# Optimization experiments

Measured on AMD Instinct MI355X. Metric: run time of the kernel, lower is better.

The kernel has to match this reference:

```python
import jax, jax.numpy as jnp
import numpy as np

B, N, DH, DG, HID, K_STEPS, CURV = 256, 2048, 128, 256, 256, 2, 1.0
SC = CURV ** 0.5
SCALE = 1.0 / (DH ** 0.5)
LN_EPS = 1e-5


def _artanh(x):
    return jnp.arctanh(jnp.clip(x, -1.0 + 1e-5, 1.0 - 1e-5))


def logmap0(x, sc=SC):
    n = jnp.maximum(jnp.linalg.norm(x, axis=-1, keepdims=True), 1e-7)
    return x * (_artanh(sc * n) / (sc * n))


def expmap0(v, sc=SC):
    n = jnp.maximum(jnp.linalg.norm(v, axis=-1, keepdims=True), 1e-7)
    return v * (jnp.tanh(sc * n) / (sc * n))


def setup_inputs() -> dict:
    key = jax.random.key(0)
    ks = jax.random.split(key, 16)

    def lin(k, out_d, in_d):
        return (jax.random.normal(k, (out_d, in_d), jnp.float32) * (in_d ** -0.5))

    demo_hyp = expmap0(0.1 * jax.random.normal(ks[0], (B, N, DH), jnp.float32))
    rho_g = jax.random.normal(ks[1], (B, DG), jnp.float32)
    return {
        "demo_hyp": demo_hyp,
        "rho_g": rho_g,
        "seed_g_w": lin(ks[2], DH, DG),
        "seed_g_b": jnp.zeros((DH,), jnp.float32),
        "seed_d_w": lin(ks[3], DH, DH),
        "pool_wq_w": lin(ks[4], DH, DH),
        "pool_wk_w": lin(ks[5], DH, DH),
        "pool_wv_w": lin(ks[6], DH, DH),
        "q_u_w": lin(ks[7], DH, DH),
        "q_g_w": lin(ks[8], DH, DG),
        "q_g_b": jnp.zeros((DH,), jnp.float32),
        "kv_w": lin(ks[9], DH, DH),
        "mlp_w1": lin(ks[10], HID, DH),
        "mlp_b1": jnp.zeros((HID,), jnp.float32),
        "mlp_w2": lin(ks[11], DH, HID),
        "mlp_b2": jnp.zeros((DH,), jnp.float32),
        "ln_g": jnp.ones((DH,), jnp.float32),
        "ln_b": jnp.zeros((DH,), jnp.float32),
    }


def reference(demo_hyp, rho_g, seed_g_w, seed_g_b, seed_d_w,
              pool_wq_w, pool_wk_w, pool_wv_w, q_u_w, q_g_w, q_g_b,
              kv_w, mlp_w1, mlp_b1, mlp_w2, mlp_b2, ln_g, ln_b):
    demo_tan = logmap0(demo_hyp)                       # (B,N,Dh)

    # seed: attention-pool demos with rho_g query
    q_seed = rho_g @ seed_g_w.T + seed_g_b             # (B,Dh)
    qk = q_seed @ pool_wq_w.T                          # (B,Dh)
    Kp = demo_tan @ pool_wk_w.T                        # (B,N,Dh)
    a = jax.nn.softmax(jnp.einsum('bd,bnd->bn', qk, Kp) * SCALE, axis=-1)
    Vp = demo_tan @ pool_wv_w.T
    pooled = jnp.einsum('bn,bnd->bd', a, Vp)           # (B,Dh)
    u = expmap0(q_seed + pooled @ seed_d_w.T)

    for _ in range(K_STEPS):
        u_tan = logmap0(u)
        mu = jnp.mean(u_tan, axis=-1, keepdims=True)
        var = jnp.var(u_tan, axis=-1, keepdims=True)
        u_tan = (u_tan - mu) * jax.lax.rsqrt(var + LN_EPS) * ln_g + ln_b
        q = u_tan @ q_u_w.T + rho_g @ q_g_w.T + q_g_b
        Kmat = demo_tan @ kv_w.T                       # keys == values
        att = jax.nn.softmax(jnp.einsum('bd,bnd->bn', q, Kmat) * SCALE, axis=-1)
        delta = jnp.einsum('bn,bnd->bd', att, Kmat)
        upd = jax.nn.gelu(delta @ mlp_w1.T + mlp_b1, approximate=False) @ mlp_w2.T + mlp_b2
        u = expmap0(u_tan + upd)
    return u
```

## Files before the change

### kernel.cpp

```cpp
#include <hip/hip_runtime.h>
#include <hip/hip_fp16.h>
#include <cstddef>
#include <cstdint>

#define B 256
#define N 2048
#define DH 128
#define DG 256
#define HID 256
#define WAVES 8
#define TPB (WAVES * 64)
#define RPI (WAVES * 8)
#define KIT (N / RPI)
#define SCALE 0.08838834764831845f
#define LN_EPS 1e-5f
#define TAN_NORM_MAX 6.2f


__device__ __forceinline__ float artanh_clip(float a) {
  a = fminf(a, 1.0f - 1e-5f);
  return 0.5f * __logf((1.0f + a) / (1.0f - a));
}

__device__ __forceinline__ float logmap_scale(float n2) {
  float nc = fmaxf(sqrtf(n2), 1e-7f);
  return artanh_clip(nc) / nc;
}

__device__ __forceinline__ float row16_sum(float x) {
  x += __int_as_float(__builtin_amdgcn_update_dpp(0, __float_as_int(x), 0x128, 0xF, 0xF, true));
  x += __int_as_float(__builtin_amdgcn_update_dpp(0, __float_as_int(x), 0x124, 0xF, 0xF, true));
  x += __int_as_float(__builtin_amdgcn_update_dpp(0, __float_as_int(x), 0x122, 0xF, 0xF, true));
  x += __int_as_float(__builtin_amdgcn_update_dpp(0, __float_as_int(x), 0x121, 0xF, 0xF, true));
  return x;
}

__device__ __forceinline__ float wave_allsum(float v) {
#pragma unroll
  for (int m = 1; m < 64; m <<= 1) v += __shfl_xor(v, m);
  return v;
}

__device__ __forceinline__ float dot128(const float* __restrict__ wrow,
                                        const float* __restrict__ x) {
  const float4* a = (const float4*)wrow;
  const float4* v = (const float4*)x;
  float s = 0.f;
#pragma unroll
  for (int j = 0; j < 32; ++j) {
    float4 u = a[j], b = v[j];
    s += u.x * b.x + u.y * b.y + u.z * b.z + u.w * b.w;
  }
  return s;
}

__device__ __forceinline__ float dot256(const float* __restrict__ wrow,
                                        const float* __restrict__ x) {
  const float4* a = (const float4*)wrow;
  const float4* v = (const float4*)x;
  float s = 0.f;
#pragma unroll
  for (int j = 0; j < 64; ++j) {
    float4 u = a[j], b = v[j];
    s += u.x * b.x + u.y * b.y + u.z * b.z + u.w * b.w;
  }
  return s;
}


__global__ __launch_bounds__(TPB, 1) void fused_refiner(
    const float* __restrict__ demo, const float* __restrict__ rho,
    const float* __restrict__ seed_g_w, const float* __restrict__ seed_g_b,
    const float* __restrict__ seed_d_w, const float* __restrict__ pool_wq_w,
    const float* __restrict__ pool_wk_w, const float* __restrict__ pool_wv_w,
    const float* __restrict__ q_u_w, const float* __restrict__ q_g_w,
    const float* __restrict__ q_g_b, const float* __restrict__ kv_w,
    const float* __restrict__ mlp_w1, const float* __restrict__ mlp_b1,
    const float* __restrict__ mlp_w2, const float* __restrict__ mlp_b2,
    const float* __restrict__ ln_g, const float* __restrict__ ln_b,
    __half* __restrict__ ycache, float* __restrict__ out) {
  const int b = blockIdx.x;
  const int tid = threadIdx.x;
  const int w = tid >> 6;
  const int lane = tid & 63;
  const int g = lane >> 4;
  const int il = lane & 15;

  __shared__ __align__(16) float s_rho[DG];
  __shared__ __align__(16) float s_x[DH];
  __shared__ __align__(16) float s_y[DH];
  __shared__ __align__(16) float s_h[HID];
  __shared__ __align__(16) float s_ut[DH];
  __shared__ __align__(16) float s_qseed[DH];
  __shared__ __align__(16) float s_qvec[DH];
  __shared__ __align__(16) float s_fold[WAVES][DH];
  __shared__ float s_l[WAVES];
  __shared__ float s_red[WAVES];
  __shared__ float s_Mb;

  auto bsumAll = [&](float v) -> float {
    v = wave_allsum(v);
    if (lane == 0) s_red[w] = v;
    __syncthreads();
    float r = s_red[0] + s_red[1] + s_red[2] + s_red[3] +
              s_red[4] + s_red[5] + s_red[6] + s_red[7];
    __syncthreads();
    return r;
  };

  auto ln_query = [&](float v) {
    float n2 = bsumAll(tid < DH ? v * v : 0.f);
    float u = 0.f, ut = 0.f;
    if (tid < DH) {
      float nc = fmaxf(sqrtf(n2), 1e-7f);
      u = v * (tanhf(nc) / nc);
    }
    float nu2 = bsumAll(tid < DH ? u * u : 0.f);
    if (tid < DH) {
      float nuc = fmaxf(sqrtf(nu2), 1e-7f);
      ut = u * (artanh_clip(nuc) / nuc);
    }
    float mu = bsumAll(tid < DH ? ut : 0.f) * (1.0f / DH);
    float d = ut - mu;
    float var = bsumAll(tid < DH ? d * d : 0.f) * (1.0f / DH);
    if (tid < DH) {
      float y = d * rsqrtf(var + LN_EPS) * ln_g[tid] + ln_b[tid];
      s_ut[tid] = y;
      s_x[tid] = y;
    }
    __syncthreads();
    if (tid < DH) {
      s_y[tid] = q_g_b[tid] + dot128(q_u_w + (size_t)tid * DH, s_x) +
                 dot256(q_g_w + (size_t)tid * DG, s_rho);
    }
    __syncthreads();
    float qp = 0.f;
    if (tid < DH) {
#pragma unroll 8
      for (int i = 0; i < DH; ++i) qp += kv_w[i * DH + tid] * s_y[i];
      s_qvec[tid] = qp;
    }
    float qn2 = bsumAll(tid < DH ? qp * qp : 0.f);
    if (tid == 0) s_Mb = SCALE * TAN_NORM_MAX * sqrtf(qn2);
    __syncthreads();
  };

  if (tid < DG) s_rho[tid] = rho[(size_t)b * DG + tid];
  __syncthreads();
  if (tid < DH) {
    float qs = seed_g_b[tid] + dot256(seed_g_w + (size_t)tid * DG, s_rho);
    s_qseed[tid] = qs;
    s_x[tid] = qs;
  }
  __syncthreads();
  if (tid < DH) s_y[tid] = dot128(pool_wq_w + (size_t)tid * DH, s_x);
  __syncthreads();
  float qp0 = 0.f;
  if (tid < DH) {
#pragma unroll 8
    for (int i = 0; i < DH; ++i) qp0 += pool_wk_w[i * DH + tid] * s_y[i];
    s_qvec[tid] = qp0;
  }
  float qn2 = bsumAll(tid < DH ? qp0 * qp0 : 0.f);
  if (tid == 0) s_Mb = SCALE * TAN_NORM_MAX * sqrtf(qn2);
  __syncthreads();

  const float* demo_b = demo + (size_t)b * N * DH;
  __half* yc_b = ycache + (size_t)b * N * DH;

  for (int pass = 0; pass < 3; ++pass) {
    const float4 qv0 = *(const float4*)&s_qvec[il * 4];
    const float4 qv1 = *(const float4*)&s_qvec[64 + il * 4];
    const float Mb = s_Mb;

    float lsum = 0.f;
    float4 accL = make_float4(0.f, 0.f, 0.f, 0.f);
    float4 accH = make_float4(0.f, 0.f, 0.f, 0.f);

    if (pass == 0) {
      const float* p = demo_b + (size_t)(w * 8 + g) * DH + il * 4;
      __half* yw = yc_b + (size_t)(w * 8 + g) * DH + (size_t)il * 8;

      float4 A1[4], A2[4], B1[4], B2[4];
#pragma unroll
      for (int j = 0; j < 3; ++j) {
        const float* pj = p + (size_t)j * RPI * DH;
        A1[j] = *(const float4*)(pj);
        A2[j] = *(const float4*)(pj + 64);
        B1[j] = *(const float4*)(pj + 4 * DH);
        B2[j] = *(const float4*)(pj + 4 * DH + 64);
      }

      for (int kk = 0; kk < KIT; kk += 4) {
#pragma unroll
        for (int j = 0; j < 4; ++j) {
          const int k = kk + j;
          const int jn = (j + 3) & 3;
          if (k + 3 < KIT) {
            const float* pn = p + (size_t)(k + 3) * RPI * DH;
            A1[jn] = *(const float4*)(pn);
            A2[jn] = *(const float4*)(pn + 64);
            B1[jn] = *(const float4*)(pn + 4 * DH);
            B2[jn] = *(const float4*)(pn + 4 * DH + 64);
          }
          float4 ca1 = A1[j], ca2 = A2[j], cb1 = B1[j], cb2 = B2[j];
          {
            float dd = qv0.x * ca1.x + qv0.y * ca1.y + qv0.z * ca1.z + qv0.w * ca1.w +
                       qv1.x * ca2.x + qv1.y * ca2.y + qv1.z * ca2.z + qv1.w * ca2.w;
            float n2 = ca1.x * ca1.x + ca1.y * ca1.y + ca1.z * ca1.z + ca1.w * ca1.w +
                       ca2.x * ca2.x + ca2.y * ca2.y + ca2.z * ca2.z + ca2.w * ca2.w;
            dd = row16_sum(dd);
            n2 = row16_sum(n2);
            float tsv = logmap_scale(n2);
            float4 y1 = make_float4(tsv * ca1.x, tsv * ca1.y, tsv * ca1.z, tsv * ca1.w);
            float4 y2 = make_float4(tsv * ca2.x, tsv * ca2.y, tsv * ca2.z, tsv * ca2.w);
            __half2 h01 = __float22half2_rn(make_float2(y1.x, y1.y));
            __half2 h23 = __float22half2_rn(make_float2(y1.z, y1.w));
            __half2 h45 = __float22half2_rn(make_float2(y2.x, y2.y));
            __half2 h67 = __float22half2_rn(make_float2(y2.z, y2.w));
            uint4 pk;
            pk.x = *(const unsigned*)&h01; pk.y = *(const unsigned*)&h23;
            pk.z = *(const unsigned*)&h45; pk.w = *(const unsigned*)&h67;
            *(uint4*)(yw + (size_t)k * RPI * DH) = pk;
            float pw = __expf(dd * tsv * SCALE - Mb);
            lsum += pw;
            accL.x += pw * y1.x; accL.y += pw * y1.y; accL.z += pw * y1.z; accL.w += pw * y1.w;
            accH.x += pw * y2.x; accH.y += pw * y2.y; accH.z += pw * y2.z; accH.w += pw * y2.w;
          }
          {
            float dd = qv0.x * cb1.x + qv0.y * cb1.y + qv0.z * cb1.z + qv0.w * cb1.w +
                       qv1.x * cb2.x + qv1.y * cb2.y + qv1.z * cb2.z + qv1.w * cb2.w;
            float n2 = cb1.x * cb1.x + cb1.y * cb1.y + cb1.z * cb1.z + cb1.w * cb1.w +
                       cb2.x * cb2.x + cb2.y * cb2.y + cb2.z * cb2.z + cb2.w * cb2.w;
            dd = row16_sum(dd);
            n2 = row16_sum(n2);
            float tsv = logmap_scale(n2);
            float4 y1 = make_float4(tsv * cb1.x, tsv * cb1.y, tsv * cb1.z, tsv * cb1.w);
            float4 y2 = make_float4(tsv * cb2.x, tsv * cb2.y, tsv * cb2.z, tsv * cb2.w);
            __half2 h01 = __float22half2_rn(make_float2(y1.x, y1.y));
            __half2 h23 = __float22half2_rn(make_float2(y1.z, y1.w));
            __half2 h45 = __float22half2_rn(make_float2(y2.x, y2.y));
            __half2 h67 = __float22half2_rn(make_float2(y2.z, y2.w));
            uint4 pk;
            pk.x = *(const unsigned*)&h01; pk.y = *(const unsigned*)&h23;
            pk.z = *(const unsigned*)&h45; pk.w = *(const unsigned*)&h67;
            *(uint4*)(yw + (size_t)k * RPI * DH + 4 * DH) = pk;
            float pw = __expf(dd * tsv * SCALE - Mb);
            lsum += pw;
            accL.x += pw * y1.x; accL.y += pw * y1.y; accL.z += pw * y1.z; accL.w += pw * y1.w;
            accH.x += pw * y2.x; accH.y += pw * y2.y; accH.z += pw * y2.z; accH.w += pw * y2.w;
          }
        }
      }
    } else {
      const __half* yr = yc_b + (size_t)(w * 8 + g) * DH + (size_t)il * 8;

      uint4 YA[4], YB[4];
#pragma unroll
      for (int j = 0; j < 3; ++j) {
        YA[j] = *(const uint4*)(yr + (size_t)j * RPI * DH);
        YB[j] = *(const uint4*)(yr + (size_t)j * RPI * DH + 4 * DH);
      }

      for (int kk = 0; kk < KIT; kk += 4) {
#pragma unroll
        for (int j = 0; j < 4; ++j) {
          const int k = kk + j;
          const int jn = (j + 3) & 3;
          if (k + 3 < KIT) {
            YA[jn] = *(const uint4*)(yr + (size_t)(k + 3) * RPI * DH);
            YB[jn] = *(const uint4*)(yr + (size_t)(k + 3) * RPI * DH + 4 * DH);
          }
          {
            uint4 pk = YA[j];
            float2 f0 = __half22float2(*(const __half2*)&pk.x);
            float2 f1 = __half22float2(*(const __half2*)&pk.y);
            float2 f2 = __half22float2(*(const __half2*)&pk.z);
            float2 f3 = __half22float2(*(const __half2*)&pk.w);
            float dd = qv0.x * f0.x + qv0.y * f0.y + qv0.z * f1.x + qv0.w * f1.y +
                       qv1.x * f2.x + qv1.y * f2.y + qv1.z * f3.x + qv1.w * f3.y;
            dd = row16_sum(dd);
            float pw = __expf(dd * SCALE - Mb);
            lsum += pw;
            accL.x += pw * f0.x; accL.y += pw * f0.y; accL.z += pw * f1.x; accL.w += pw * f1.y;
            accH.x += pw * f2.x; accH.y += pw * f2.y; accH.z += pw * f3.x; accH.w += pw * f3.y;
          }
          {
            uint4 pk = YB[j];
            float2 f0 = __half22float2(*(const __half2*)&pk.x);
            float2 f1 = __half22float2(*(const __half2*)&pk.y);
            float2 f2 = __half22float2(*(const __half2*)&pk.z);
            float2 f3 = __half22float2(*(const __half2*)&pk.w);
            float dd = qv0.x * f0.x + qv0.y * f0.y + qv0.z * f1.x + qv0.w * f1.y +
                       qv1.x * f2.x + qv1.y * f2.y + qv1.z * f3.x + qv1.w * f3.y;
            dd = row16_sum(dd);
            float pw = __expf(dd * SCALE - Mb);
            lsum += pw;
            accL.x += pw * f0.x; accL.y += pw * f0.y; accL.z += pw * f1.x; accL.w += pw * f1.y;
            accH.x += pw * f2.x; accH.y += pw * f2.y; accH.z += pw * f3.x; accH.w += pw * f3.y;
          }
        }
      }
    }

    accL.x += __shfl_xor(accL.x, 16); accL.x += __shfl_xor(accL.x, 32);
    accL.y += __shfl_xor(accL.y, 16); accL.y += __shfl_xor(accL.y, 32);
    accL.z += __shfl_xor(accL.z, 16); accL.z += __shfl_xor(accL.z, 32);
    accL.w += __shfl_xor(accL.w, 16); accL.w += __shfl_xor(accL.w, 32);
    accH.x += __shfl_xor(accH.x, 16); accH.x += __shfl_xor(accH.x, 32);
    accH.y += __shfl_xor(accH.y, 16); accH.y += __shfl_xor(accH.y, 32);
    accH.z += __shfl_xor(accH.z, 16); accH.z += __shfl_xor(accH.z, 32);
    accH.w += __shfl_xor(accH.w, 16); accH.w += __shfl_xor(accH.w, 32);
    lsum += __shfl_xor(lsum, 16); lsum += __shfl_xor(lsum, 32);
    if (g == 0) {
      *(float4*)&s_fold[w][il * 4] = accL;
      *(float4*)&s_fold[w][64 + il * 4] = accH;
      if (il == 0) s_l[w] = lsum;
    }
    __syncthreads();

    if (tid < DH) {
      float a = 0.f;
#pragma unroll
      for (int j = 0; j < WAVES; ++j) a += s_fold[j][tid];
      float L = s_l[0] + s_l[1] + s_l[2] + s_l[3] +
                s_l[4] + s_l[5] + s_l[6] + s_l[7];
      s_x[tid] = a / L;
    }
    __syncthreads();

    if (pass == 0) {
      if (tid < DH) s_y[tid] = dot128(pool_wv_w + (size_t)tid * DH, s_x);
      __syncthreads();
      float v = 0.f;
      if (tid < DH) v = s_qseed[tid] + dot128(seed_d_w + (size_t)tid * DH, s_y);
      ln_query(v);
    } else {
      if (tid < DH) s_y[tid] = dot128(kv_w + (size_t)tid * DH, s_x);
      __syncthreads();
      if (tid < HID) {
        float h = mlp_b1[tid] + dot128(mlp_w1 + (size_t)tid * DH, s_y);
        s_h[tid] = 0.5f * h * (1.0f + erff(h * 0.70710678118654752f));
      }
      __syncthreads();
      float v = 0.f;
      if (tid < DH)
        v = s_ut[tid] + mlp_b2[tid] + dot256(mlp_w2 + (size_t)tid * HID, s_h);
      if (pass == 2) {
        float n2 = bsumAll(tid < DH ? v * v : 0.f);
        if (tid < DH) {
          float nc = fmaxf(sqrtf(n2), 1e-7f);
          out[(size_t)b * DH + tid] = v * (tanhf(nc) / nc);
        }
      } else {
        ln_query(v);
      }
    }
  }
}


extern "C" void kernel_launch(void* const* d_in, const int* in_sizes, int n_in,
                              void* d_out, int out_size, void* d_ws, size_t ws_size,
                              hipStream_t stream) {
  const float* demo      = (const float*)d_in[0];
  const float* rho       = (const float*)d_in[1];
  const float* seed_g_w  = (const float*)d_in[2];
  const float* seed_g_b  = (const float*)d_in[3];
  const float* seed_d_w  = (const float*)d_in[4];
  const float* pool_wq_w = (const float*)d_in[5];
  const float* pool_wk_w = (const float*)d_in[6];
  const float* pool_wv_w = (const float*)d_in[7];
  const float* q_u_w     = (const float*)d_in[8];
  const float* q_g_w     = (const float*)d_in[9];
  const float* q_g_b     = (const float*)d_in[10];
  const float* kv_w      = (const float*)d_in[11];
  const float* mlp_w1    = (const float*)d_in[12];
  const float* mlp_b1    = (const float*)d_in[13];
  const float* mlp_w2    = (const float*)d_in[14];
  const float* mlp_b2    = (const float*)d_in[15];
  const float* ln_g      = (const float*)d_in[16];
  const float* ln_b      = (const float*)d_in[17];
  float* out = (float*)d_out;
  __half* ycache = (__half*)d_ws;
  (void)ws_size; (void)in_sizes; (void)n_in; (void)out_size;

  fused_refiner<<<B, TPB, 0, stream>>>(demo, rho, seed_g_w, seed_g_b, seed_d_w,
                                       pool_wq_w, pool_wk_w, pool_wv_w, q_u_w,
                                       q_g_w, q_g_b, kv_w, mlp_w1, mlp_b1,
                                       mlp_w2, mlp_b2, ln_g, ln_b, ycache, out);
}
```

Baseline: 519.3 us.

## Double waves per block and shrink register prefetch to one-ahead

Raises the block from 8 to 16 waves (1024 threads) with launch bounds allowing more occupancy, and replaces the 3-deep register prefetch ring with a single-iteration lookahead. Each wave now streams half as many rows, and more waves per CU are meant to hide memory latency through parallelism instead of explicit prefetch. The cost is a larger cross-wave reduction, more threads idle during the small matvec phases, and tighter register limits.

```diff
diff --git a/kernel.cpp b/kernel.cpp
--- a/kernel.cpp
+++ b/kernel.cpp
@@ -8,7 +8,7 @@
 #define DH 128
 #define DG 256
 #define HID 256
-#define WAVES 8
+#define WAVES 16
 #define TPB (WAVES * 64)
 #define RPI (WAVES * 8)
 #define KIT (N / RPI)
@@ -68,7 +68,7 @@
 }
 
 
-__global__ __launch_bounds__(TPB, 1) void fused_refiner(
+__global__ __launch_bounds__(TPB, 4) void fused_refiner(
     const float* __restrict__ demo, const float* __restrict__ rho,
     const float* __restrict__ seed_g_w, const float* __restrict__ seed_g_b,
     const float* __restrict__ seed_d_w, const float* __restrict__ pool_wq_w,
@@ -102,8 +102,9 @@
     v = wave_allsum(v);
     if (lane == 0) s_red[w] = v;
     __syncthreads();
-    float r = s_red[0] + s_red[1] + s_red[2] + s_red[3] +
-              s_red[4] + s_red[5] + s_red[6] + s_red[7];
+    float r = 0.f;
+#pragma unroll
+    for (int j = 0; j < WAVES; ++j) r += s_red[j];
     __syncthreads();
     return r;
   };
@@ -181,124 +182,104 @@
       const float* p = demo_b + (size_t)(w * 8 + g) * DH + il * 4;
       __half* yw = yc_b + (size_t)(w * 8 + g) * DH + (size_t)il * 8;
 
-      float4 A1[4], A2[4], B1[4], B2[4];
-#pragma unroll
-      for (int j = 0; j < 3; ++j) {
-        const float* pj = p + (size_t)j * RPI * DH;
-        A1[j] = *(const float4*)(pj);
-        A2[j] = *(const float4*)(pj + 64);
-        B1[j] = *(const float4*)(pj + 4 * DH);
-        B2[j] = *(const float4*)(pj + 4 * DH + 64);
-      }
-
-      for (int kk = 0; kk < KIT; kk += 4) {
-#pragma unroll
-        for (int j = 0; j < 4; ++j) {
-          const int k = kk + j;
-          const int jn = (j + 3) & 3;
-          if (k + 3 < KIT) {
-            const float* pn = p + (size_t)(k + 3) * RPI * DH;
-            A1[jn] = *(const float4*)(pn);
-            A2[jn] = *(const float4*)(pn + 64);
-            B1[jn] = *(const float4*)(pn + 4 * DH);
-            B2[jn] = *(const float4*)(pn + 4 * DH + 64);
-          }
-          float4 ca1 = A1[j], ca2 = A2[j], cb1 = B1[j], cb2 = B2[j];
-          {
-            float dd = qv0.x * ca1.x + qv0.y * ca1.y + qv0.z * ca1.z + qv0.w * ca1.w +
-                       qv1.x * ca2.x + qv1.y * ca2.y + qv1.z * ca2.z + qv1.w * ca2.w;
-            float n2 = ca1.x * ca1.x + ca1.y * ca1.y + ca1.z * ca1.z + ca1.w * ca1.w +
-                       ca2.x * ca2.x + ca2.y * ca2.y + ca2.z * ca2.z + ca2.w * ca2.w;
-            dd = row16_sum(dd);
-            n2 = row16_sum(n2);
-            float tsv = logmap_scale(n2);
-            float4 y1 = make_float4(tsv * ca1.x, tsv * ca1.y, tsv * ca1.z, tsv * ca1.w);
-            float4 y2 = make_float4(tsv * ca2.x, tsv * ca2.y, tsv * ca2.z, tsv * ca2.w);
-            __half2 h01 = __float22half2_rn(make_float2(y1.x, y1.y));
-            __half2 h23 = __float22half2_rn(make_float2(y1.z, y1.w));
-            __half2 h45 = __float22half2_rn(make_float2(y2.x, y2.y));
-            __half2 h67 = __float22half2_rn(make_float2(y2.z, y2.w));
-            uint4 pk;
-            pk.x = *(const unsigned*)&h01; pk.y = *(const unsigned*)&h23;
-            pk.z = *(const unsigned*)&h45; pk.w = *(const unsigned*)&h67;
-            *(uint4*)(yw + (size_t)k * RPI * DH) = pk;
-            float pw = __expf(dd * tsv * SCALE - Mb);
-            lsum += pw;
-            accL.x += pw * y1.x; accL.y += pw * y1.y; accL.z += pw * y1.z; accL.w += pw * y1.w;
-            accH.x += pw * y2.x; accH.y += pw * y2.y; accH.z += pw * y2.z; accH.w += pw * y2.w;
-          }
-          {
-            float dd = qv0.x * cb1.x + qv0.y * cb1.y + qv0.z * cb1.z + qv0.w * cb1.w +
-                       qv1.x * cb2.x + qv1.y * cb2.y + qv1.z * cb2.z + qv1.w * cb2.w;
-            float n2 = cb1.x * cb1.x + cb1.y * cb1.y + cb1.z * cb1.z + cb1.w * cb1.w +
-                       cb2.x * cb2.x + cb2.y * cb2.y + cb2.z * cb2.z + cb2.w * cb2.w;
-            dd = row16_sum(dd);
-            n2 = row16_sum(n2);
-            float tsv = logmap_scale(n2);
-            float4 y1 = make_float4(tsv * cb1.x, tsv * cb1.y, tsv * cb1.z, tsv * cb1.w);
-            float4 y2 = make_float4(tsv * cb2.x, tsv * cb2.y, tsv * cb2.z, tsv * cb2.w);
-            __half2 h01 = __float22half2_rn(make_float2(y1.x, y1.y));
-            __half2 h23 = __float22half2_rn(make_float2(y1.z, y1.w));
-            __half2 h45 = __float22half2_rn(make_float2(y2.x, y2.y));
-            __half2 h67 = __float22half2_rn(make_float2(y2.z, y2.w));
-            uint4 pk;
-            pk.x = *(const unsigned*)&h01; pk.y = *(const unsigned*)&h23;
-            pk.z = *(const unsigned*)&h45; pk.w = *(const unsigned*)&h67;
-            *(uint4*)(yw + (size_t)k * RPI * DH + 4 * DH) = pk;
-            float pw = __expf(dd * tsv * SCALE - Mb);
-            lsum += pw;
-            accL.x += pw * y1.x; accL.y += pw * y1.y; accL.z += pw * y1.z; accL.w += pw * y1.w;
-            accH.x += pw * y2.x; accH.y += pw * y2.y; accH.z += pw * y2.z; accH.w += pw * y2.w;
-          }
+      float4 xa1 = *(const float4*)(p);
+      float4 xa2 = *(const float4*)(p + 64);
+      float4 xb1 = *(const float4*)(p + 4 * DH);
+      float4 xb2 = *(const float4*)(p + 4 * DH + 64);
+
+      for (int k = 0; k < KIT; ++k) {
+        float4 ca1 = xa1, ca2 = xa2, cb1 = xb1, cb2 = xb2;
+        if (k + 1 < KIT) {
+          const float* pn = p + (size_t)(k + 1) * RPI * DH;
+          xa1 = *(const float4*)(pn);
+          xa2 = *(const float4*)(pn + 64);
+          xb1 = *(const float4*)(pn + 4 * DH);
+          xb2 = *(const float4*)(pn + 4 * DH + 64);
+        }
+        {
+          float dd = qv0.x * ca1.x + qv0.y * ca1.y + qv0.z * ca1.z + qv0.w * ca1.w +
+                     qv1.x * ca2.x + qv1.y * ca2.y + qv1.z * ca2.z + qv1.w * ca2.w;
+          float n2 = ca1.x * ca1.x + ca1.y * ca1.y + ca1.z * ca1.z + ca1.w * ca1.w +
+                     ca2.x * ca2.x + ca2.y * ca2.y + ca2.z * ca2.z + ca2.w * ca2.w;
+          dd = row16_sum(dd);
+          n2 = row16_sum(n2);
+          float tsv = logmap_scale(n2);
+          float4 y1 = make_float4(tsv * ca1.x, tsv * ca1.y, tsv * ca1.z, tsv * ca1.w);
+          float4 y2 = make_float4(tsv * ca2.x, tsv * ca2.y, tsv * ca2.z, tsv * ca2.w);
+          __half2 h01 = __float22half2_rn(make_float2(y1.x, y1.y));
+          __half2 h23 = __float22half2_rn(make_float2(y1.z, y1.w));
+          __half2 h45 = __float22half2_rn(make_float2(y2.x, y2.y));
+          __half2 h67 = __float22half2_rn(make_float2(y2.z, y2.w));
+          uint4 pk;
+          pk.x = *(const unsigned*)&h01; pk.y = *(const unsigned*)&h23;
+          pk.z = *(const unsigned*)&h45; pk.w = *(const unsigned*)&h67;
+          *(uint4*)(yw + (size_t)k * RPI * DH) = pk;
+          float pw = __expf(dd * tsv * SCALE - Mb);
+          lsum += pw;
+          accL.x += pw * y1.x; accL.y += pw * y1.y; accL.z += pw * y1.z; accL.w += pw * y1.w;
+          accH.x += pw * y2.x; accH.y += pw * y2.y; accH.z += pw * y2.z; accH.w += pw * y2.w;
+        }
+        {
+          float dd = qv0.x * cb1.x + qv0.y * cb1.y + qv0.z * cb1.z + qv0.w * cb1.w +
+                     qv1.x * cb2.x + qv1.y * cb2.y + qv1.z * cb2.z + qv1.w * cb2.w;
+          float n2 = cb1.x * cb1.x + cb1.y * cb1.y + cb1.z * cb1.z + cb1.w * cb1.w +
+                     cb2.x * cb2.x + cb2.y * cb2.y + cb2.z * cb2.z + cb2.w * cb2.w;
+          dd = row16_sum(dd);
+          n2 = row16_sum(n2);
+          float tsv = logmap_scale(n2);
+          float4 y1 = make_float4(tsv * cb1.x, tsv * cb1.y, tsv * cb1.z, tsv * cb1.w);
+          float4 y2 = make_float4(tsv * cb2.x, tsv * cb2.y, tsv * cb2.z, tsv * cb2.w);
+          __half2 h01 = __float22half2_rn(make_float2(y1.x, y1.y));
+          __half2 h23 = __float22half2_rn(make_float2(y1.z, y1.w));
+          __half2 h45 = __float22half2_rn(make_float2(y2.x, y2.y));
+          __half2 h67 = __float22half2_rn(make_float2(y2.z, y2.w));
+          uint4 pk;
+          pk.x = *(const unsigned*)&h01; pk.y = *(const unsigned*)&h23;
+          pk.z = *(const unsigned*)&h45; pk.w = *(const unsigned*)&h67;
+          *(uint4*)(yw + (size_t)k * RPI * DH + 4 * DH) = pk;
+          float pw = __expf(dd * tsv * SCALE - Mb);
+          lsum += pw;
+          accL.x += pw * y1.x; accL.y += pw * y1.y; accL.z += pw * y1.z; accL.w += pw * y1.w;
+          accH.x += pw * y2.x; accH.y += pw * y2.y; accH.z += pw * y2.z; accH.w += pw * y2.w;
         }
       }
     } else {
       const __half* yr = yc_b + (size_t)(w * 8 + g) * DH + (size_t)il * 8;
 
-      uint4 YA[4], YB[4];
-#pragma unroll
-      for (int j = 0; j < 3; ++j) {
-        YA[j] = *(const uint4*)(yr + (size_t)j * RPI * DH);
-        YB[j] = *(const uint4*)(yr + (size_t)j * RPI * DH + 4 * DH);
-      }
-
-      for (int kk = 0; kk < KIT; kk += 4) {
-#pragma unroll
-        for (int j = 0; j < 4; ++j) {
-          const int k = kk + j;
-          const int jn = (j + 3) & 3;
-          if (k + 3 < KIT) {
-            YA[jn] = *(const uint4*)(yr + (size_t)(k + 3) * RPI * DH);
-            YB[jn] = *(const uint4*)(yr + (size_t)(k + 3) * RPI * DH + 4 * DH);
-          }
-          {
-            uint4 pk = YA[j];
-            float2 f0 = __half22float2(*(const __half2*)&pk.x);
-            float2 f1 = __half22float2(*(const __half2*)&pk.y);
-            float2 f2 = __half22float2(*(const __half2*)&pk.z);
-            float2 f3 = __half22float2(*(const __half2*)&pk.w);
-            float dd = qv0.x * f0.x + qv0.y * f0.y + qv0.z * f1.x + qv0.w * f1.y +
-                       qv1.x * f2.x + qv1.y * f2.y + qv1.z * f3.x + qv1.w * f3.y;
-            dd = row16_sum(dd);
-            float pw = __expf(dd * SCALE - Mb);
-            lsum += pw;
-            accL.x += pw * f0.x; accL.y += pw * f0.y; accL.z += pw * f1.x; accL.w += pw * f1.y;
-            accH.x += pw * f2.x; accH.y += pw * f2.y; accH.z += pw * f3.x; accH.w += pw * f3.y;
-          }
-          {
-            uint4 pk = YB[j];
-            float2 f0 = __half22float2(*(const __half2*)&pk.x);
-            float2 f1 = __half22float2(*(const __half2*)&pk.y);
-            float2 f2 = __half22float2(*(const __half2*)&pk.z);
-            float2 f3 = __half22float2(*(const __half2*)&pk.w);
-            float dd = qv0.x * f0.x + qv0.y * f0.y + qv0.z * f1.x + qv0.w * f1.y +
-                       qv1.x * f2.x + qv1.y * f2.y + qv1.z * f3.x + qv1.w * f3.y;
-            dd = row16_sum(dd);
-            float pw = __expf(dd * SCALE - Mb);
-            lsum += pw;
-            accL.x += pw * f0.x; accL.y += pw * f0.y; accL.z += pw * f1.x; accL.w += pw * f1.y;
-            accH.x += pw * f2.x; accH.y += pw * f2.y; accH.z += pw * f3.x; accH.w += pw * f3.y;
-          }
+      uint4 ya = *(const uint4*)(yr);
+      uint4 yb = *(const uint4*)(yr + 4 * DH);
+
+      for (int k = 0; k < KIT; ++k) {
+        uint4 cya = ya, cyb = yb;
+        if (k + 1 < KIT) {
+          ya = *(const uint4*)(yr + (size_t)(k + 1) * RPI * DH);
+          yb = *(const uint4*)(yr + (size_t)(k + 1) * RPI * DH + 4 * DH);
+        }
+        {
+          float2 f0 = __half22float2(*(const __half2*)&cya.x);
+          float2 f1 = __half22float2(*(const __half2*)&cya.y);
+          float2 f2 = __half22float2(*(const __half2*)&cya.z);
+          float2 f3 = __half22float2(*(const __half2*)&cya.w);
+          float dd = qv0.x * f0.x + qv0.y * f0.y + qv0.z * f1.x + qv0.w * f1.y +
+                     qv1.x * f2.x + qv1.y * f2.y + qv1.z * f3.x + qv1.w * f3.y;
+          dd = row16_sum(dd);
+          float pw = __expf(dd * SCALE - Mb);
+          lsum += pw;
+          accL.x += pw * f0.x; accL.y += pw * f0.y; accL.z += pw * f1.x; accL.w += pw * f1.y;
+          accH.x += pw * f2.x; accH.y += pw * f2.y; accH.z += pw * f3.x; accH.w += pw * f3.y;
+        }
+        {
+          float2 f0 = __half22float2(*(const __half2*)&cyb.x);
+          float2 f1 = __half22float2(*(const __half2*)&cyb.y);
+          float2 f2 = __half22float2(*(const __half2*)&cyb.z);
+          float2 f3 = __half22float2(*(const __half2*)&cyb.w);
+          float dd = qv0.x * f0.x + qv0.y * f0.y + qv0.z * f1.x + qv0.w * f1.y +
+                     qv1.x * f2.x + qv1.y * f2.y + qv1.z * f3.x + qv1.w * f3.y;
+          dd = row16_sum(dd);
+          float pw = __expf(dd * SCALE - Mb);
+          lsum += pw;
+          accL.x += pw * f0.x; accL.y += pw * f0.y; accL.z += pw * f1.x; accL.w += pw * f1.y;
+          accH.x += pw * f2.x; accH.y += pw * f2.y; accH.z += pw * f3.x; accH.w += pw * f3.y;
         }
       }
     }
@@ -323,8 +304,9 @@
       float a = 0.f;
 #pragma unroll
       for (int j = 0; j < WAVES; ++j) a += s_fold[j][tid];
-      float L = s_l[0] + s_l[1] + s_l[2] + s_l[3] +
-                s_l[4] + s_l[5] + s_l[6] + s_l[7];
+      float L = 0.f;
+#pragma unroll
+      for (int j = 0; j < WAVES; ++j) L += s_l[j];
       s_x[tid] = a / L;
     }
     __syncthreads();
```

After: 537.7 us. 1.04x slower.
